# Performance work log

Measured on AMD Instinct MI355X. Metric: run time of the kernel, lower is better.

The kernel has to match this reference:

```python
import jax, jax.numpy as jnp
import numpy as np

B, S, D, L, V = 2, 2048, 1024, 4, 32000
EXP = 4  # ContinuumMemoryBlock expansion
EPS = 1e-5  # torch LayerNorm default eps


def _layernorm(x, g, b):
    m = x.mean(-1, keepdims=True)
    v = x.var(-1, keepdims=True)  # biased, matches torch LayerNorm
    return (x - m) * jax.lax.rsqrt(v + EPS) * g + b


def setup_inputs() -> dict:
    key = jax.random.key(0)
    ks = jax.random.split(key, 12)
    w = lambda k, shape: jax.random.normal(k, shape, jnp.float32) * 0.02
    return {
        "x": jax.random.normal(ks[0], (B, S, D), jnp.float32),
        # SelfModifyingLayer projections (stored as [in, out]; y = x @ W + b)
        "Wq": w(ks[1], (D, D)), "bq": jnp.zeros((D,), jnp.float32),
        "Wk": w(ks[2], (D, D)), "bk": jnp.zeros((D,), jnp.float32),
        "Wv": w(ks[3], (D, D)), "bv": jnp.zeros((D,), jnp.float32),
        "Wo": w(ks[4], (D, D)), "bo": jnp.zeros((D,), jnp.float32),
        "decay_param": jnp.asarray(0.0, jnp.float32),
        "g_fast": jnp.ones((D,), jnp.float32), "b_fast": jnp.zeros((D,), jnp.float32),
        # stacked CMS layers
        "W1": w(ks[5], (L, D, EXP * D)), "b1": jnp.zeros((L, EXP * D), jnp.float32),
        "W2": w(ks[6], (L, EXP * D, D)), "b2": jnp.zeros((L, D), jnp.float32),
        "g_cms": jnp.ones((L, D), jnp.float32), "beta_cms": jnp.zeros((L, D), jnp.float32),
        # LM head
        "Wh": w(ks[7], (D, V)), "bh": jnp.zeros((V,), jnp.float32),
    }


def reference(x, Wq, bq, Wk, bk, Wv, bv, Wo, bo, decay_param, g_fast, b_fast,
              W1, b1, W2, b2, g_cms, beta_cms, Wh, bh):
    # --- SelfModifyingLayer (fast-weight linear attention) ---
    q = x @ Wq + bq                      # [B,S,D]
    k = jax.nn.elu(x @ Wk + bk) + 1.0    # [B,S,D], positive keys
    v = x @ Wv + bv                      # [B,S,D]
    decay = jax.nn.sigmoid(decay_param)
    # Closed form of: M_t = decay*M_{t-1} + k_t^T v_t, out_t = q_t @ M_{t-1}
    #   out_t = sum_{s<t} decay^(t-1-s) (q_t . k_s) v_s
    idx = jnp.arange(x.shape[1])
    expo = idx[:, None] - idx[None, :] - 1          # t - s - 1
    decay_mask = jnp.where(expo >= 0,
                           decay ** jnp.maximum(expo, 0).astype(jnp.float32),
                           0.0)                      # [S,S], strictly causal
    scores = jnp.einsum('bqd,bkd->bqk', q, k) * decay_mask
    fast = jnp.einsum('bqk,bkd->bqd', scores, v) @ Wo + bo
    # --- residual + norm ---
    h = _layernorm(x + fast, g_fast, b_fast)
    # --- ContinuumMemoryBlock stack (Dropout in eval mode -> identity) ---
    def cms(h, p):
        Wa, ba, Wb, bb, g, be = p
        y = jax.nn.gelu(h @ Wa + ba, approximate=False) @ Wb + bb
        return _layernorm(h + y, g, be), None
    h, _ = jax.lax.scan(cms, h, (W1, b1, W2, b2, g_cms, beta_cms))
    # --- LM head ---
    return h @ Wh + bh  # [B,S,V]
```

## Files before the change

kernel.cpp:

```cpp
#include <hip/hip_runtime.h>
#include <cstdint>

typedef __bf16 bf16;
typedef bf16 bf16x8 __attribute__((ext_vector_type(8)));
typedef bf16 bf16x4 __attribute__((ext_vector_type(4)));
typedef float f32x4 __attribute__((ext_vector_type(4)));
typedef __attribute__((address_space(1))) uint32_t gu32;
typedef __attribute__((address_space(3))) uint32_t lu32;

#define DEV static __device__ __forceinline__

DEV void gl_lds16(const bf16* g, bf16* l) {
  __builtin_amdgcn_global_load_lds((const gu32*)g, (lu32*)l, 16, 0, 0);
}

__global__ void k_pow(const float* __restrict__ dp, float* __restrict__ powd) {
  const int i = blockIdx.x * 256 + threadIdx.x;
  if (i < 2048) {
    const float decay = 1.0f / (1.0f + expf(-dp[0]));
    powd[i] = powf(decay, (float)i);
  }
}

__global__ __launch_bounds__(256) void k_convA(const float* __restrict__ src,
                                               bf16* __restrict__ dh,
                                               bf16* __restrict__ dl, int K) {
  const int Kc = K >> 3;
  const int kc0 = blockIdx.x * 8;
  const int mblk = blockIdx.y;
  const int t = threadIdx.x;
  const int kcl = t & 7;
  const int r0 = t >> 3;
#pragma unroll
  for (int ri = 0; ri < 4; ++ri) {
    const int row = ri * 32 + r0;
    const float* p = src + (size_t)(mblk * 128 + row) * K + (size_t)(kc0 + kcl) * 8;
    const float4 a = *(const float4*)p;
    const float4 b = *(const float4*)(p + 4);
    const float v[8] = {a.x, a.y, a.z, a.w, b.x, b.y, b.z, b.w};
    bf16x8 h, l;
#pragma unroll
    for (int j = 0; j < 8; ++j) {
      const bf16 hj = (bf16)v[j];
      h[j] = hj;
      l[j] = (bf16)(v[j] - (float)hj);
    }
    const size_t off = ((size_t)(mblk * Kc + kc0 + kcl) * 128 + row) * 8;
    *(bf16x8*)(dh + off) = h;
    *(bf16x8*)(dl + off) = l;
  }
}

__global__ __launch_bounds__(256) void k_convB(const float* __restrict__ src,
                                               bf16* __restrict__ dh,
                                               bf16* __restrict__ dl, int K, int N,
                                               long long sbat, long long dbat) {
  src += (long long)blockIdx.z * sbat;
  dh += (long long)blockIdx.z * dbat;
  dl += (long long)blockIdx.z * dbat;
  const int Kc = K >> 3;
  const int kc0 = blockIdx.x * 8;
  const int nblk = blockIdx.y;
  const int t = threadIdx.x;
  const int c = t & 127;
  const int h2 = t >> 7;
#pragma unroll
  for (int it = 0; it < 4; ++it) {
    const int kcl = it * 2 + h2;
    const int kb = (kc0 + kcl) * 8;
    float v[8];
#pragma unroll
    for (int j = 0; j < 8; ++j) v[j] = src[(size_t)(kb + j) * N + nblk * 128 + c];
    bf16x8 h, l;
#pragma unroll
    for (int j = 0; j < 8; ++j) {
      const bf16 hj = (bf16)v[j];
      h[j] = hj;
      l[j] = (bf16)(v[j] - (float)hj);
    }
    const size_t off = ((size_t)(nblk * Kc + kc0 + kcl) * 128 + c) * 8;
    *(bf16x8*)(dh + off) = h;
    *(bf16x8*)(dl + off) = l;
  }
}

template <int EPI, bool TOUT>
__global__ __launch_bounds__(256, 2) void k_gemm(
    const bf16* __restrict__ Ah, const bf16* __restrict__ Al,
    const bf16* __restrict__ Bh, const bf16* __restrict__ Bl,
    float* __restrict__ C, bf16* __restrict__ Dh, bf16* __restrict__ Dl,
    const float* __restrict__ bias, const float* __restrict__ powd,
    int N, int K, int kband,
    long long abat, long long bbat, long long cbat) {
  const int mblk = blockIdx.x;
  const int nblk = blockIdx.y;
  if (EPI == 3 && nblk > mblk) return;

  Ah += (long long)blockIdx.z * abat;
  Al += (long long)blockIdx.z * abat;
  Bh += (long long)blockIdx.z * bbat;
  Bl += (long long)blockIdx.z * bbat;
  C += (long long)blockIdx.z * cbat;
  Dh += (long long)blockIdx.z * cbat;
  Dl += (long long)blockIdx.z * cbat;

  const int tid = threadIdx.x;
  const int lane = tid & 63;
  const int wave = tid >> 6;
  const int wm = (wave >> 1) * 64;
  const int wn = (wave & 1) * 64;
  const int kg = lane >> 4;
  const int rr = lane & 15;

  __shared__ __align__(16) bf16 sAh[4096], sAl[4096], sBh[4096], sBl[4096];

  const size_t aBase = (size_t)mblk * K * 128 + (size_t)tid * 8;
  const size_t bBase = (size_t)nblk * K * 128 + (size_t)tid * 8;

  f32x4 acc[4][4];
  const f32x4 zero = {0.0f, 0.0f, 0.0f, 0.0f};
#pragma unroll
  for (int m = 0; m < 4; ++m)
#pragma unroll
    for (int n = 0; n < 4; ++n) acc[m][n] = zero;

  int nk = K >> 5;
  if (kband) {
    const int cap = (mblk + 1) * kband;
    nk = nk < cap ? nk : cap;
  }
  for (int kt = 0; kt < nk; ++kt) {
    const size_t ga = aBase + (size_t)kt * 4096;
    const size_t gb = bBase + (size_t)kt * 4096;
    gl_lds16(Ah + ga, sAh + tid * 8);
    gl_lds16(Ah + ga + 2048, sAh + 2048 + tid * 8);
    gl_lds16(Al + ga, sAl + tid * 8);
    gl_lds16(Al + ga + 2048, sAl + 2048 + tid * 8);
    gl_lds16(Bh + gb, sBh + tid * 8);
    gl_lds16(Bh + gb + 2048, sBh + 2048 + tid * 8);
    gl_lds16(Bl + gb, sBl + tid * 8);
    gl_lds16(Bl + gb + 2048, sBl + 2048 + tid * 8);
    __syncthreads();

    bf16x8 fah[4], fal[4], fbh[4], fbl[4];
#pragma unroll
    for (int m = 0; m < 4; ++m) {
      const int off = (kg * 128 + wm + m * 16 + rr) * 8;
      fah[m] = *(const bf16x8*)(sAh + off);
      fal[m] = *(const bf16x8*)(sAl + off);
    }
#pragma unroll
    for (int n = 0; n < 4; ++n) {
      const int off = (kg * 128 + wn + n * 16 + rr) * 8;
      fbh[n] = *(const bf16x8*)(sBh + off);
      fbl[n] = *(const bf16x8*)(sBl + off);
    }
#pragma unroll
    for (int m = 0; m < 4; ++m)
#pragma unroll
      for (int n = 0; n < 4; ++n) {
        acc[m][n] = __builtin_amdgcn_mfma_f32_16x16x32_bf16(fah[m], fbh[n], acc[m][n], 0, 0, 0);
        acc[m][n] = __builtin_amdgcn_mfma_f32_16x16x32_bf16(fah[m], fbl[n], acc[m][n], 0, 0, 0);
        acc[m][n] = __builtin_amdgcn_mfma_f32_16x16x32_bf16(fal[m], fbh[n], acc[m][n], 0, 0, 0);
      }
    __syncthreads();
  }

  const int Kc2 = N >> 3;
#pragma unroll
  for (int n = 0; n < 4; ++n) {
    const int gcol = nblk * 128 + wn + n * 16 + rr;
    const float bv = bias ? bias[gcol] : 0.0f;
    const size_t tb = ((size_t)(mblk * Kc2 + (gcol >> 3)) * 128) * 8 + (gcol & 7);
#pragma unroll
    for (int m = 0; m < 4; ++m) {
#pragma unroll
      for (int j = 0; j < 4; ++j) {
        const int r = wm + kg * 4 + m * 16 + j;
        float x = acc[m][n][j] + bv;
        if (EPI == 1) x = (x > 0.0f) ? x + 1.0f : expf(x);
        if (EPI == 2) x = 0.5f * x * (1.0f + erff(x * 0.70710678118654752f));
        if (EPI == 3) {
          const int e = (mblk * 128 + r) - gcol - 1;
          x = (e >= 0) ? x * powd[e] : 0.0f;
        }
        if (!TOUT) {
          C[(size_t)(mblk * 128 + r) * N + gcol] = x;
        } else {
          const bf16 h = (bf16)x;
          Dh[tb + (size_t)r * 8] = h;
          Dl[tb + (size_t)r * 8] = (bf16)(x - (float)h);
        }
      }
    }
  }
}

__global__ __launch_bounds__(256) void k_ln(const float* x1, const float* x2,
                                            const float* g, const float* be,
                                            float* out, bf16* th, bf16* tl) {
  const int row = blockIdx.x;
  const int t = threadIdx.x;
  const int lane = t & 63;
  const int wave = t >> 6;
  const float4 a = *(const float4*)(x1 + (size_t)row * 1024 + t * 4);
  const float4 b = *(const float4*)(x2 + (size_t)row * 1024 + t * 4);
  float v[4] = {a.x + b.x, a.y + b.y, a.z + b.z, a.w + b.w};
  __shared__ float red[4];
  float s = v[0] + v[1] + v[2] + v[3];
#pragma unroll
  for (int o = 1; o < 64; o <<= 1) s += __shfl_xor(s, o);
  if (lane == 0) red[wave] = s;
  __syncthreads();
  s = red[0] + red[1] + red[2] + red[3];
  const float mean = s * (1.0f / 1024.0f);
  float q = 0.0f;
#pragma unroll
  for (int j = 0; j < 4; ++j) {
    const float d = v[j] - mean;
    q += d * d;
  }
#pragma unroll
  for (int o = 1; o < 64; o <<= 1) q += __shfl_xor(q, o);
  __syncthreads();
  if (lane == 0) red[wave] = q;
  __syncthreads();
  q = red[0] + red[1] + red[2] + red[3];
  const float rstd = rsqrtf(q * (1.0f / 1024.0f) + 1e-5f);
  const int cc = t * 4;
  float y[4];
#pragma unroll
  for (int j = 0; j < 4; ++j) y[j] = (v[j] - mean) * rstd * g[cc + j] + be[cc + j];
  const float4 o4 = {y[0], y[1], y[2], y[3]};
  *(float4*)(out + (size_t)row * 1024 + cc) = o4;
  const int mblk = row >> 7, r = row & 127, kc = t >> 1, j0 = (t & 1) * 4;
  const size_t off = ((size_t)(mblk * 128 + kc) * 128 + r) * 8 + j0;
  bf16x4 hh, ll;
#pragma unroll
  for (int j = 0; j < 4; ++j) {
    const bf16 hj = (bf16)y[j];
    hh[j] = hj;
    ll[j] = (bf16)(y[j] - (float)hj);
  }
  *(bf16x4*)(th + off) = hh;
  *(bf16x4*)(tl + off) = ll;
}

extern "C" void kernel_launch(void* const* d_in, const int* in_sizes, int n_in,
                              void* d_out, int out_size, void* d_ws, size_t ws_size,
                              hipStream_t stream) {
  const float* x = (const float*)d_in[0];
  const float* Wq = (const float*)d_in[1];
  const float* bq = (const float*)d_in[2];
  const float* Wk = (const float*)d_in[3];
  const float* bk = (const float*)d_in[4];
  const float* Wv = (const float*)d_in[5];
  const float* bv = (const float*)d_in[6];
  const float* Wo = (const float*)d_in[7];
  const float* bo = (const float*)d_in[8];
  const float* dp = (const float*)d_in[9];
  const float* gf = (const float*)d_in[10];
  const float* bfv = (const float*)d_in[11];
  const float* W1 = (const float*)d_in[12];
  const float* b1 = (const float*)d_in[13];
  const float* W2 = (const float*)d_in[14];
  const float* b2 = (const float*)d_in[15];
  const float* gc = (const float*)d_in[16];
  const float* bc = (const float*)d_in[17];
  const float* Wh = (const float*)d_in[18];
  const float* bh = (const float*)d_in[19];
  float* out = (float*)d_out;

  char* w = (char*)d_ws;
  size_t o = 0;
  auto alloc = [&](size_t bytes) -> void* {
    void* p = w + o;
    o += (bytes + 255) & ~(size_t)255;
    return p;
  };
  const size_t MD = (size_t)4096 * 1024;
  float* powd = (float*)alloc(2048 * 4);
  bf16* XAh = (bf16*)alloc(MD * 2);
  bf16* XAl = (bf16*)alloc(MD * 2);
  bf16* Wqh = (bf16*)alloc((size_t)1024 * 1024 * 2);
  bf16* Wql = (bf16*)alloc((size_t)1024 * 1024 * 2);
  bf16* Wkh = (bf16*)alloc((size_t)1024 * 1024 * 2);
  bf16* Wkl = (bf16*)alloc((size_t)1024 * 1024 * 2);
  bf16* Wvh = (bf16*)alloc((size_t)1024 * 1024 * 2);
  bf16* Wvl = (bf16*)alloc((size_t)1024 * 1024 * 2);
  bf16* Woh = (bf16*)alloc((size_t)1024 * 1024 * 2);
  bf16* Wol = (bf16*)alloc((size_t)1024 * 1024 * 2);
  float* vf = (float*)alloc(MD * 4);
  bf16* vTh = (bf16*)alloc(MD * 2);
  bf16* vTl = (bf16*)alloc(MD * 2);
  bf16* SCh = (bf16*)alloc((size_t)2 * 2048 * 2048 * 2);
  bf16* SCl = (bf16*)alloc((size_t)2 * 2048 * 2048 * 2);
  bf16* AHh = (bf16*)alloc((size_t)4096 * 4096 * 2);
  bf16* AHl = (bf16*)alloc((size_t)4096 * 4096 * 2);
  bf16* BHh = (bf16*)alloc((size_t)32000 * 1024 * 2);
  bf16* BHl = (bf16*)alloc((size_t)32000 * 1024 * 2);
  float* hf = (float*)alloc(MD * 4);
  float* t1 = (float*)alloc(MD * 4);
  float* t2 = (float*)alloc(MD * 4);
  bf16* hAh = (bf16*)alloc(MD * 2);
  bf16* hAl = (bf16*)alloc(MD * 2);

  const long long SD = 2048LL * 1024;
  const long long SS = 2048LL * 2048;
  float* nullf = nullptr;
  bf16* nullb = nullptr;

  k_pow<<<8, 256, 0, stream>>>(dp, powd);

  k_convA<<<dim3(16, 32), 256, 0, stream>>>(x, XAh, XAl, 1024);
  k_convB<<<dim3(16, 8), 256, 0, stream>>>(Wq, Wqh, Wql, 1024, 1024, 0, 0);
  k_convB<<<dim3(16, 8), 256, 0, stream>>>(Wk, Wkh, Wkl, 1024, 1024, 0, 0);
  k_convB<<<dim3(16, 8), 256, 0, stream>>>(Wv, Wvh, Wvl, 1024, 1024, 0, 0);
  k_convB<<<dim3(16, 8), 256, 0, stream>>>(Wo, Woh, Wol, 1024, 1024, 0, 0);
  k_gemm<0, true><<<dim3(32, 8), 256, 0, stream>>>(XAh, XAl, Wqh, Wql, nullf, AHh, AHl,
                                                   bq, nullptr, 1024, 1024, 0, 0, 0, 0);
  k_gemm<1, true><<<dim3(32, 8), 256, 0, stream>>>(XAh, XAl, Wkh, Wkl, nullf, BHh, BHl,
                                                   bk, nullptr, 1024, 1024, 0, 0, 0, 0);
  k_gemm<0, false><<<dim3(32, 8), 256, 0, stream>>>(XAh, XAl, Wvh, Wvl, vf, nullb, nullb,
                                                    bv, nullptr, 1024, 1024, 0, 0, 0, 0);
  k_convB<<<dim3(32, 8, 2), 256, 0, stream>>>(vf, vTh, vTl, 2048, 1024, SD, SD);

  k_gemm<3, true><<<dim3(16, 16, 2), 256, 0, stream>>>(AHh, AHl, BHh, BHl, nullf, SCh, SCl,
                                                       nullptr, powd, 2048, 1024, 0, SD, SD, SS);
  k_gemm<0, true><<<dim3(16, 8, 2), 256, 0, stream>>>(SCh, SCl, vTh, vTl, nullf, AHh, AHl,
                                                      nullptr, nullptr, 1024, 2048, 4, SS, SD, SD);
  k_gemm<0, false><<<dim3(32, 8), 256, 0, stream>>>(AHh, AHl, Woh, Wol, t2, nullb, nullb,
                                                    bo, nullptr, 1024, 1024, 0, 0, 0, 0);
  k_ln<<<4096, 256, 0, stream>>>(x, t2, gf, bfv, hf, hAh, hAl);

  for (int l = 0; l < 4; ++l) {
    k_convB<<<dim3(16, 32), 256, 0, stream>>>(W1 + (size_t)l * 1024 * 4096, BHh, BHl, 1024, 4096, 0, 0);
    k_gemm<2, true><<<dim3(32, 32), 256, 0, stream>>>(hAh, hAl, BHh, BHl, nullf, AHh, AHl,
                                                      b1 + l * 4096, nullptr, 4096, 1024, 0, 0, 0, 0);
    k_convB<<<dim3(64, 8), 256, 0, stream>>>(W2 + (size_t)l * 4096 * 1024, BHh, BHl, 4096, 1024, 0, 0);
    k_gemm<0, false><<<dim3(32, 8), 256, 0, stream>>>(AHh, AHl, BHh, BHl, t1, nullb, nullb,
                                                      b2 + l * 1024, nullptr, 1024, 4096, 0, 0, 0, 0);
    k_ln<<<4096, 256, 0, stream>>>(hf, t1, gc + l * 1024, bc + l * 1024, hf, hAh, hAl);
  }

  k_convB<<<dim3(16, 250), 256, 0, stream>>>(Wh, BHh, BHl, 1024, 32000, 0, 0);
  k_gemm<0, false><<<dim3(32, 250), 256, 0, stream>>>(hAh, hAl, BHh, BHl, out, nullb, nullb,
                                                      bh, nullptr, 32000, 1024, 0, 0, 0, 0);
}
```

Baseline: 2.622 ms.

## Fuse QKV GEMMs, add split-K for narrow GEMMs, XCD-aware block remap

The Q, K and V projections now run as one 3072-wide GEMM whose epilogue picks the bias, the ELU+1 step and the output buffer per column. The Wo projection and CMS down-projection GEMMs use split-K over 2 or 4 z-slices, writing partial sums that the LayerNorm kernel adds together along with the bias. This raises the workgroup count on these 256-block GEMMs. Large grids (768 or more workgroups) get an XCD-aware block index remap to improve L2 locality. The cost is extra fp32 partial-sum traffic and a scratch buffer reorganised into one allocation.

```diff
diff --git a/kernel.cpp b/kernel.cpp
--- a/kernel.cpp
+++ b/kernel.cpp
@@ -84,25 +84,40 @@
   }
 }
 
-template <int EPI, bool TOUT>
+template <int EPI, bool TOUT, bool SPLITK>
 __global__ __launch_bounds__(256, 2) void k_gemm(
     const bf16* __restrict__ Ah, const bf16* __restrict__ Al,
     const bf16* __restrict__ Bh, const bf16* __restrict__ Bl,
     float* __restrict__ C, bf16* __restrict__ Dh, bf16* __restrict__ Dl,
-    const float* __restrict__ bias, const float* __restrict__ powd,
+    bf16* __restrict__ Dh2, bf16* __restrict__ Dl2,
+    const float* __restrict__ bias, const float* __restrict__ bias2,
+    const float* __restrict__ bias3, const float* __restrict__ powd,
     int N, int K, int kband,
     long long abat, long long bbat, long long cbat) {
-  const int mblk = blockIdx.x;
-  const int nblk = blockIdx.y;
+  int mblk = blockIdx.x;
+  int nblk = blockIdx.y;
+  const int nwg = (int)(gridDim.x * gridDim.y);
+  if (nwg >= 768) {
+    int id = (int)(blockIdx.y * gridDim.x + blockIdx.x);
+    const int q = nwg >> 3, r = nwg & 7;
+    const int xcd = id & 7, rank = id >> 3;
+    id = (xcd < r ? xcd * (q + 1) : r * (q + 1) + (xcd - r) * q) + rank;
+    mblk = id % (int)gridDim.x;
+    nblk = id / (int)gridDim.x;
+  }
   if (EPI == 3 && nblk > mblk) return;
 
-  Ah += (long long)blockIdx.z * abat;
-  Al += (long long)blockIdx.z * abat;
-  Bh += (long long)blockIdx.z * bbat;
-  Bl += (long long)blockIdx.z * bbat;
-  C += (long long)blockIdx.z * cbat;
-  Dh += (long long)blockIdx.z * cbat;
-  Dl += (long long)blockIdx.z * cbat;
+  if (SPLITK) {
+    C += (long long)blockIdx.z * cbat;
+  } else {
+    Ah += (long long)blockIdx.z * abat;
+    Al += (long long)blockIdx.z * abat;
+    Bh += (long long)blockIdx.z * bbat;
+    Bl += (long long)blockIdx.z * bbat;
+    C += (long long)blockIdx.z * cbat;
+    Dh += (long long)blockIdx.z * cbat;
+    Dl += (long long)blockIdx.z * cbat;
+  }
 
   const int tid = threadIdx.x;
   const int lane = tid & 63;
@@ -124,12 +139,18 @@
 #pragma unroll
     for (int n = 0; n < 4; ++n) acc[m][n] = zero;
 
+  int kt0 = 0;
   int nk = K >> 5;
+  if (SPLITK) {
+    const int per = nk / (int)gridDim.z;
+    kt0 = (int)blockIdx.z * per;
+    nk = kt0 + per;
+  }
   if (kband) {
     const int cap = (mblk + 1) * kband;
     nk = nk < cap ? nk : cap;
   }
-  for (int kt = 0; kt < nk; ++kt) {
+  for (int kt = kt0; kt < nk; ++kt) {
     const size_t ga = aBase + (size_t)kt * 4096;
     const size_t gb = bBase + (size_t)kt * 4096;
     gl_lds16(Ah + ga, sAh + tid * 8);
@@ -166,46 +187,82 @@
     __syncthreads();
   }
 
+  const int row0 = wm + kg * 4;
   const int Kc2 = N >> 3;
 #pragma unroll
   for (int n = 0; n < 4; ++n) {
     const int gcol = nblk * 128 + wn + n * 16 + rr;
-    const float bv = bias ? bias[gcol] : 0.0f;
-    const size_t tb = ((size_t)(mblk * Kc2 + (gcol >> 3)) * 128) * 8 + (gcol & 7);
-#pragma unroll
-    for (int m = 0; m < 4; ++m) {
-#pragma unroll
-      for (int j = 0; j < 4; ++j) {
-        const int r = wm + kg * 4 + m * 16 + j;
-        float x = acc[m][n][j] + bv;
-        if (EPI == 1) x = (x > 0.0f) ? x + 1.0f : expf(x);
-        if (EPI == 2) x = 0.5f * x * (1.0f + erff(x * 0.70710678118654752f));
-        if (EPI == 3) {
-          const int e = (mblk * 128 + r) - gcol - 1;
-          x = (e >= 0) ? x * powd[e] : 0.0f;
+    if (EPI == 4) {
+      const int sel = gcol >> 10;
+      const int lcol = gcol & 1023;
+      const float bv = (sel == 0 ? bias : sel == 1 ? bias2 : bias3)[lcol];
+      bf16* dh = sel ? Dh2 : Dh;
+      bf16* dl = sel ? Dl2 : Dl;
+      const size_t tb = ((size_t)(mblk * 128 + (lcol >> 3)) * 128) * 8 + (lcol & 7);
+#pragma unroll
+      for (int m = 0; m < 4; ++m)
+#pragma unroll
+        for (int j = 0; j < 4; ++j) {
+          const int r = row0 + m * 16 + j;
+          float xv = acc[m][n][j] + bv;
+          if (sel == 1) xv = (xv > 0.0f) ? xv + 1.0f : expf(xv);
+          if (sel == 2) {
+            C[(size_t)(mblk * 128 + r) * 1024 + lcol] = xv;
+          } else {
+            const bf16 h = (bf16)xv;
+            dh[tb + (size_t)r * 8] = h;
+            dl[tb + (size_t)r * 8] = (bf16)(xv - (float)h);
+          }
         }
-        if (!TOUT) {
-          C[(size_t)(mblk * 128 + r) * N + gcol] = x;
-        } else {
-          const bf16 h = (bf16)x;
-          Dh[tb + (size_t)r * 8] = h;
-          Dl[tb + (size_t)r * 8] = (bf16)(x - (float)h);
+    } else {
+      const float bv = bias ? bias[gcol] : 0.0f;
+      const size_t tb = ((size_t)(mblk * Kc2 + (gcol >> 3)) * 128) * 8 + (gcol & 7);
+#pragma unroll
+      for (int m = 0; m < 4; ++m)
+#pragma unroll
+        for (int j = 0; j < 4; ++j) {
+          const int r = row0 + m * 16 + j;
+          float xv = acc[m][n][j] + bv;
+          if (EPI == 2) xv = 0.5f * xv * (1.0f + erff(xv * 0.70710678118654752f));
+          if (EPI == 3) {
+            const int e = (mblk * 128 + r) - gcol - 1;
+            xv = (e >= 0) ? xv * powd[e] : 0.0f;
+          }
+          if (!TOUT) {
+            C[(size_t)(mblk * 128 + r) * N + gcol] = xv;
+          } else {
+            const bf16 h = (bf16)xv;
+            Dh[tb + (size_t)r * 8] = h;
+            Dl[tb + (size_t)r * 8] = (bf16)(xv - (float)h);
+          }
         }
-      }
     }
   }
 }
 
-__global__ __launch_bounds__(256) void k_ln(const float* x1, const float* x2,
-                                            const float* g, const float* be,
-                                            float* out, bf16* th, bf16* tl) {
+__global__ __launch_bounds__(256) void k_ln(const float* __restrict__ x1,
+                                            const float* __restrict__ x2, int nparts,
+                                            long long pstride,
+                                            const float* __restrict__ bias2,
+                                            const float* __restrict__ g,
+                                            const float* __restrict__ be,
+                                            float* __restrict__ out,
+                                            bf16* __restrict__ th, bf16* __restrict__ tl) {
   const int row = blockIdx.x;
   const int t = threadIdx.x;
   const int lane = t & 63;
   const int wave = t >> 6;
-  const float4 a = *(const float4*)(x1 + (size_t)row * 1024 + t * 4);
-  const float4 b = *(const float4*)(x2 + (size_t)row * 1024 + t * 4);
-  float v[4] = {a.x + b.x, a.y + b.y, a.z + b.z, a.w + b.w};
+  const int cc = t * 4;
+  const float4 a = *(const float4*)(x1 + (size_t)row * 1024 + cc);
+  float v[4] = {a.x, a.y, a.z, a.w};
+  for (int p = 0; p < nparts; ++p) {
+    const float4 b = *(const float4*)(x2 + (size_t)p * pstride + (size_t)row * 1024 + cc);
+    v[0] += b.x; v[1] += b.y; v[2] += b.z; v[3] += b.w;
+  }
+  if (bias2) {
+    const float4 b = *(const float4*)(bias2 + cc);
+    v[0] += b.x; v[1] += b.y; v[2] += b.z; v[3] += b.w;
+  }
   __shared__ float red[4];
   float s = v[0] + v[1] + v[2] + v[3];
 #pragma unroll
@@ -227,7 +284,6 @@
   __syncthreads();
   q = red[0] + red[1] + red[2] + red[3];
   const float rstd = rsqrtf(q * (1.0f / 1024.0f) + 1e-5f);
-  const int cc = t * 4;
   float y[4];
 #pragma unroll
   for (int j = 0; j < 4; ++j) y[j] = (v[j] - mean) * rstd * g[cc + j] + be[cc + j];
@@ -279,71 +335,89 @@
     return p;
   };
   const size_t MD = (size_t)4096 * 1024;
+
   float* powd = (float*)alloc(2048 * 4);
-  bf16* XAh = (bf16*)alloc(MD * 2);
-  bf16* XAl = (bf16*)alloc(MD * 2);
-  bf16* Wqh = (bf16*)alloc((size_t)1024 * 1024 * 2);
-  bf16* Wql = (bf16*)alloc((size_t)1024 * 1024 * 2);
-  bf16* Wkh = (bf16*)alloc((size_t)1024 * 1024 * 2);
-  bf16* Wkl = (bf16*)alloc((size_t)1024 * 1024 * 2);
-  bf16* Wvh = (bf16*)alloc((size_t)1024 * 1024 * 2);
-  bf16* Wvl = (bf16*)alloc((size_t)1024 * 1024 * 2);
-  bf16* Woh = (bf16*)alloc((size_t)1024 * 1024 * 2);
-  bf16* Wol = (bf16*)alloc((size_t)1024 * 1024 * 2);
-  float* vf = (float*)alloc(MD * 4);
-  bf16* vTh = (bf16*)alloc(MD * 2);
-  bf16* vTl = (bf16*)alloc(MD * 2);
-  bf16* SCh = (bf16*)alloc((size_t)2 * 2048 * 2048 * 2);
-  bf16* SCl = (bf16*)alloc((size_t)2 * 2048 * 2048 * 2);
-  bf16* AHh = (bf16*)alloc((size_t)4096 * 4096 * 2);
-  bf16* AHl = (bf16*)alloc((size_t)4096 * 4096 * 2);
-  bf16* BHh = (bf16*)alloc((size_t)32000 * 1024 * 2);
-  bf16* BHl = (bf16*)alloc((size_t)32000 * 1024 * 2);
   float* hf = (float*)alloc(MD * 4);
-  float* t1 = (float*)alloc(MD * 4);
-  float* t2 = (float*)alloc(MD * 4);
+  float* t1 = (float*)alloc(MD * 4 * 4);
+  float* t2 = (float*)alloc(MD * 4 * 2);
   bf16* hAh = (bf16*)alloc(MD * 2);
   bf16* hAl = (bf16*)alloc(MD * 2);
+  char* sb = (char*)alloc((size_t)(65536 + 32768) * 1024 * 2 * 2);
+  bf16* BHh = (bf16*)sb;
+  bf16* BHl = BHh + (size_t)32000 * 1024;
+  bf16* AHh = BHl + (size_t)32000 * 1024;
+  bf16* AHl = AHh + (size_t)4096 * 4096;
+  size_t so = 0;
+  auto salloc = [&](size_t bytes) -> void* {
+    void* p = sb + so;
+    so += (bytes + 255) & ~(size_t)255;
+    return p;
+  };
+  bf16* XAh = (bf16*)salloc(MD * 2);
+  bf16* XAl = (bf16*)salloc(MD * 2);
+  bf16* WQKVh = (bf16*)salloc((size_t)3072 * 1024 * 2);
+  bf16* WQKVl = (bf16*)salloc((size_t)3072 * 1024 * 2);
+  bf16* Woh = (bf16*)salloc((size_t)1024 * 1024 * 2);
+  bf16* Wol = (bf16*)salloc((size_t)1024 * 1024 * 2);
+  float* vf = (float*)salloc(MD * 4);
+  bf16* vTh = (bf16*)salloc(MD * 2);
+  bf16* vTl = (bf16*)salloc(MD * 2);
+  bf16* QTh = (bf16*)salloc(MD * 2);
+  bf16* QTl = (bf16*)salloc(MD * 2);
+  bf16* KTh = (bf16*)salloc(MD * 2);
+  bf16* KTl = (bf16*)salloc(MD * 2);
+  bf16* SCh = (bf16*)salloc((size_t)2 * 2048 * 2048 * 2);
+  bf16* SCl = (bf16*)salloc((size_t)2 * 2048 * 2048 * 2);
+  bf16* FAh = (bf16*)salloc(MD * 2);
+  bf16* FAl = (bf16*)salloc(MD * 2);
 
   const long long SD = 2048LL * 1024;
   const long long SS = 2048LL * 2048;
-  float* nullf = nullptr;
-  bf16* nullb = nullptr;
+  const long long PD = 4096LL * 1024;
+  const size_t SL = (size_t)1024 * 1024;
+  float* nf = nullptr;
+  bf16* nb = nullptr;
 
   k_pow<<<8, 256, 0, stream>>>(dp, powd);
 
   k_convA<<<dim3(16, 32), 256, 0, stream>>>(x, XAh, XAl, 1024);
-  k_convB<<<dim3(16, 8), 256, 0, stream>>>(Wq, Wqh, Wql, 1024, 1024, 0, 0);
-  k_convB<<<dim3(16, 8), 256, 0, stream>>>(Wk, Wkh, Wkl, 1024, 1024, 0, 0);
-  k_convB<<<dim3(16, 8), 256, 0, stream>>>(Wv, Wvh, Wvl, 1024, 1024, 0, 0);
+  k_convB<<<dim3(16, 8), 256, 0, stream>>>(Wq, WQKVh, WQKVl, 1024, 1024, 0, 0);
+  k_convB<<<dim3(16, 8), 256, 0, stream>>>(Wk, WQKVh + SL, WQKVl + SL, 1024, 1024, 0, 0);
+  k_convB<<<dim3(16, 8), 256, 0, stream>>>(Wv, WQKVh + 2 * SL, WQKVl + 2 * SL, 1024, 1024, 0, 0);
   k_convB<<<dim3(16, 8), 256, 0, stream>>>(Wo, Woh, Wol, 1024, 1024, 0, 0);
-  k_gemm<0, true><<<dim3(32, 8), 256, 0, stream>>>(XAh, XAl, Wqh, Wql, nullf, AHh, AHl,
-                                                   bq, nullptr, 1024, 1024, 0, 0, 0, 0);
-  k_gemm<1, true><<<dim3(32, 8), 256, 0, stream>>>(XAh, XAl, Wkh, Wkl, nullf, BHh, BHl,
-                                                   bk, nullptr, 1024, 1024, 0, 0, 0, 0);
-  k_gemm<0, false><<<dim3(32, 8), 256, 0, stream>>>(XAh, XAl, Wvh, Wvl, vf, nullb, nullb,
-                                                    bv, nullptr, 1024, 1024, 0, 0, 0, 0);
+  k_gemm<4, false, false><<<dim3(32, 24), 256, 0, stream>>>(
+      XAh, XAl, WQKVh, WQKVl, vf, QTh, QTl, KTh, KTl, bq, bk, bv, nullptr,
+      3072, 1024, 0, 0, 0, 0);
   k_convB<<<dim3(32, 8, 2), 256, 0, stream>>>(vf, vTh, vTl, 2048, 1024, SD, SD);
 
-  k_gemm<3, true><<<dim3(16, 16, 2), 256, 0, stream>>>(AHh, AHl, BHh, BHl, nullf, SCh, SCl,
-                                                       nullptr, powd, 2048, 1024, 0, SD, SD, SS);
-  k_gemm<0, true><<<dim3(16, 8, 2), 256, 0, stream>>>(SCh, SCl, vTh, vTl, nullf, AHh, AHl,
-                                                      nullptr, nullptr, 1024, 2048, 4, SS, SD, SD);
-  k_gemm<0, false><<<dim3(32, 8), 256, 0, stream>>>(AHh, AHl, Woh, Wol, t2, nullb, nullb,
-                                                    bo, nullptr, 1024, 1024, 0, 0, 0, 0);
-  k_ln<<<4096, 256, 0, stream>>>(x, t2, gf, bfv, hf, hAh, hAl);
+  k_gemm<3, true, false><<<dim3(16, 16, 2), 256, 0, stream>>>(
+      QTh, QTl, KTh, KTl, nf, SCh, SCl, nb, nb, nullptr, nullptr, nullptr, powd,
+      2048, 1024, 0, SD, SD, SS);
+  k_gemm<0, true, false><<<dim3(16, 8, 2), 256, 0, stream>>>(
+      SCh, SCl, vTh, vTl, nf, FAh, FAl, nb, nb, nullptr, nullptr, nullptr, nullptr,
+      1024, 2048, 4, SS, SD, SD);
+  k_gemm<0, false, true><<<dim3(32, 8, 2), 256, 0, stream>>>(
+      FAh, FAl, Woh, Wol, t2, nb, nb, nb, nb, nullptr, nullptr, nullptr, nullptr,
+      1024, 1024, 0, 0, 0, PD);
+  k_ln<<<4096, 256, 0, stream>>>(x, t2, 2, PD, bo, gf, bfv, hf, hAh, hAl);
 
   for (int l = 0; l < 4; ++l) {
-    k_convB<<<dim3(16, 32), 256, 0, stream>>>(W1 + (size_t)l * 1024 * 4096, BHh, BHl, 1024, 4096, 0, 0);
-    k_gemm<2, true><<<dim3(32, 32), 256, 0, stream>>>(hAh, hAl, BHh, BHl, nullf, AHh, AHl,
-                                                      b1 + l * 4096, nullptr, 4096, 1024, 0, 0, 0, 0);
-    k_convB<<<dim3(64, 8), 256, 0, stream>>>(W2 + (size_t)l * 4096 * 1024, BHh, BHl, 4096, 1024, 0, 0);
-    k_gemm<0, false><<<dim3(32, 8), 256, 0, stream>>>(AHh, AHl, BHh, BHl, t1, nullb, nullb,
-                                                      b2 + l * 1024, nullptr, 1024, 4096, 0, 0, 0, 0);
-    k_ln<<<4096, 256, 0, stream>>>(hf, t1, gc + l * 1024, bc + l * 1024, hf, hAh, hAl);
+    k_convB<<<dim3(16, 32), 256, 0, stream>>>(W1 + (size_t)l * 1024 * 4096, BHh, BHl,
+                                              1024, 4096, 0, 0);
+    k_gemm<2, true, false><<<dim3(32, 32), 256, 0, stream>>>(
+        hAh, hAl, BHh, BHl, nf, AHh, AHl, nb, nb, b1 + l * 4096, nullptr, nullptr,
+        nullptr, 4096, 1024, 0, 0, 0, 0);
+    k_convB<<<dim3(64, 8), 256, 0, stream>>>(W2 + (size_t)l * 4096 * 1024, BHh, BHl,
+                                             4096, 1024, 0, 0);
+    k_gemm<0, false, true><<<dim3(32, 8, 4), 256, 0, stream>>>(
+        AHh, AHl, BHh, BHl, t1, nb, nb, nb, nb, nullptr, nullptr, nullptr, nullptr,
+        1024, 4096, 0, 0, 0, PD);
+    k_ln<<<4096, 256, 0, stream>>>(hf, t1, 4, PD, b2 + l * 1024, gc + l * 1024,
+                                   bc + l * 1024, hf, hAh, hAl);
   }
 
   k_convB<<<dim3(16, 250), 256, 0, stream>>>(Wh, BHh, BHl, 1024, 32000, 0, 0);
-  k_gemm<0, false><<<dim3(32, 250), 256, 0, stream>>>(hAh, hAl, BHh, BHl, out, nullb, nullb,
-                                                      bh, nullptr, 32000, 1024, 0, 0, 0, 0);
-}
+  k_gemm<0, false, false><<<dim3(32, 250), 256, 0, stream>>>(
+      hAh, hAl, BHh, BHl, out, nb, nb, nb, nb, bh, nullptr, nullptr, nullptr,
+      32000, 1024, 0, 0, 0, 0);
+}
```

Result: faster. 2.460 ms (-6.2%).
